# Kernel optimization log

Measured on AMD Instinct MI355X. Metric: run time of the kernel, lower is better.

## Reference

```python
import jax, jax.numpy as jnp
import numpy as np

B, S, D, O, R, E = 2, 4096, 4096, 4096, 256, 8
SCALE = 2.0

def setup_inputs() -> dict:
    key = jax.random.key(0)
    k_x, k_t, k_w, k_a, k_b = jax.random.split(key, 5)
    x = jax.random.normal(k_x, (B, S, D), dtype=jnp.float32)
    token_type = jax.random.randint(k_t, (S,), 0, E, dtype=jnp.int64)
    # weight_base: [out_features, in_features] as required by F.linear
    weight_base = jax.random.normal(k_w, (O, D), dtype=jnp.float32) * 0.02
    # LoRA stacks: lora_A [E, D, R], lora_B [E, R, O]. (Original inits B to zeros;
    # we use small random values so the LoRA path is numerically non-trivial.)
    lora_A = jax.random.normal(k_a, (E, D, R), dtype=jnp.float32) * 0.02
    lora_B = jax.random.normal(k_b, (E, R, O), dtype=jnp.float32) * 0.02
    return {"x": x, "weight_base": weight_base, "lora_A": lora_A,
            "lora_B": lora_B, "token_type": token_type}

def reference(x, weight_base, lora_A, lora_B, token_type):
    # base GEMM: F.linear(x, W) = x @ W.T  -> [B, S, O]
    base = jnp.einsum('bsd,od->bso', x, weight_base)
    # per-expert low-rank projection: h[e,b,s,:] = x[b,s,:] @ lora_A[e]
    h = jnp.einsum('bsd,edr->ebsr', x, lora_A)              # [E, B, S, R]
    # dispatch: zero out tokens not routed to expert e (token_type partitions S)
    onehot = jax.nn.one_hot(token_type, E, dtype=x.dtype)   # [S, E]
    h = h * onehot.T[:, None, :, None]                      # mask over (e, s)
    # combine: sum over experts of masked h @ lora_B[e]
    lora = jnp.einsum('ebsr,ero->bso', h, lora_B)           # [B, S, O]
    # every token has token_type in [0, E), so scatter covers all positions:
    # result = base + scale * expert_lora everywhere
    return base + SCALE * lora
```

## Files before the change

### kernel.cpp

```cpp
#include <hip/hip_runtime.h>

#define S_TOK 4096
#define D_DIM 4096
#define O_DIM 4096
#define R_DIM 256
#define E_EXP 8
#define NTOK  8192
#define KSPLIT 4

typedef __bf16 bf16x8 __attribute__((ext_vector_type(8)));
typedef float  f32x4  __attribute__((ext_vector_type(4)));

__device__ __forceinline__ unsigned short f2bf(float f) {
  unsigned int u = __float_as_uint(f);
  u += 0x7FFFu + ((u >> 16) & 1u);
  return (unsigned short)(u >> 16);
}
__device__ __forceinline__ float bf2f(unsigned short h) {
  return __uint_as_float(((unsigned int)h) << 16);
}

__device__ __forceinline__ void gload_lds16(const unsigned short* g, unsigned short* l) {
  __builtin_amdgcn_global_load_lds((const __attribute__((address_space(1))) void*)g,
                                   (__attribute__((address_space(3))) void*)l, 16, 0, 0);
}

#define PIPE_FENCE(N)                                                        \
  do {                                                                       \
    asm volatile("s_waitcnt vmcnt(" #N ")\n\ts_barrier" ::: "memory");       \
    __builtin_amdgcn_sched_barrier(0);                                       \
  } while (0)
#define LGKMC(N)                                                             \
  do {                                                                       \
    asm volatile("s_waitcnt lgkmcnt(" #N ")" ::: "memory");                  \
    __builtin_amdgcn_sched_barrier(0);                                       \
  } while (0)
#define SBAR0 __builtin_amdgcn_sched_barrier(0)

__global__ void cast8(const float* __restrict__ in, unsigned short* __restrict__ out) {
  size_t g = (size_t)blockIdx.x * 256 + threadIdx.x;
  const float4* i4 = (const float4*)in;
  float4 a = i4[g * 2], b = i4[g * 2 + 1];
  union { unsigned short h[8]; int4 v; } u;
  u.h[0] = f2bf(a.x); u.h[1] = f2bf(a.y); u.h[2] = f2bf(a.z); u.h[3] = f2bf(a.w);
  u.h[4] = f2bf(b.x); u.h[5] = f2bf(b.y); u.h[6] = f2bf(b.z); u.h[7] = f2bf(b.w);
  ((int4*)out)[g] = u.v;
}

__global__ void transpose_cast(const float* __restrict__ in, unsigned short* __restrict__ out,
                               int P, int Q) {
  __shared__ unsigned short tile[32][33];
  int e = blockIdx.z;
  int pt = blockIdx.x * 32, qt = blockIdx.y * 32;
  const float* ie = in + (size_t)e * P * Q;
  unsigned short* oe = out + (size_t)e * P * Q;
  int tx = threadIdx.x & 31, ty = threadIdx.x >> 5;
  #pragma unroll
  for (int i = 0; i < 32; i += 8) {
    int p = pt + ty + i, q = qt + tx;
    tile[ty + i][tx] = f2bf(ie[(size_t)p * Q + q]);
  }
  __syncthreads();
  #pragma unroll
  for (int i = 0; i < 32; i += 8) {
    int q = qt + ty + i, p = pt + tx;
    oe[(size_t)q * P + p] = tile[tx][ty + i];
  }
}

__global__ void sort_tokens(const int* __restrict__ tt, int* __restrict__ token_perm,
                            int* __restrict__ inv_perm,
                            int* __restrict__ tile_e, int* __restrict__ tile_j0,
                            int* __restrict__ tile_jend, int* __restrict__ ntiles_out) {
  __shared__ int ltt[S_TOK];
  __shared__ int lc[256 * 8];
  __shared__ int basee[8], cnte[8];
  __shared__ int ssl[S_TOK];
  int t = threadIdx.x;
  for (int s = t; s < S_TOK; s += 256) ltt[s] = tt[s];
  __syncthreads();
  int c[8] = {0,0,0,0,0,0,0,0};
  #pragma unroll
  for (int i = 0; i < 16; i++) { int e = ltt[t * 16 + i]; c[e]++; }
  #pragma unroll
  for (int e = 0; e < 8; e++) lc[t * 8 + e] = c[e];
  __syncthreads();
  if (t < 8) {
    int run = 0;
    for (int q = 0; q < 256; q++) { int tmp = lc[q * 8 + t]; lc[q * 8 + t] = run; run += tmp; }
    cnte[t] = run;
  }
  __syncthreads();
  if (t == 0) { int tot = 0; for (int e = 0; e < 8; e++) { basee[e] = tot; tot += cnte[e]; } }
  __syncthreads();
  int off[8];
  #pragma unroll
  for (int e = 0; e < 8; e++) off[e] = basee[e] + lc[t * 8 + e];
  #pragma unroll
  for (int i = 0; i < 16; i++) { int s = t * 16 + i; int e = ltt[s]; ssl[off[e]++] = s; }
  __syncthreads();
  for (int j = t; j < NTOK; j += 256) {
    int row = ((j & 1) << 12) + ssl[j >> 1];
    token_perm[j] = row;
    inv_perm[row] = j;
  }
  if (t == 0) {
    int nt = 0;
    for (int e = 0; e < 8; e++) {
      int js = 2 * basee[e], je = js + 2 * cnte[e];
      for (int j0 = js; j0 < je; j0 += 128) {
        tile_e[nt] = e; tile_j0[nt] = j0;
        tile_jend[nt] = (je < j0 + 128) ? je : (j0 + 128);
        nt++;
      }
    }
    *ntiles_out = nt;
  }
}

template<int FUSED>
__global__ __launch_bounds__(512, 2) void gemm256_dense(
    const unsigned short* __restrict__ A, const unsigned short* __restrict__ B,
    float* __restrict__ C, const unsigned short* __restrict__ lout,
    const int* __restrict__ invp) {
  __shared__ __align__(16) unsigned short ldsA[2][2][8192];
  __shared__ __align__(16) unsigned short ldsB[2][2][8192];
  int b = blockIdx.x;
  int xc = b & 7, q = b >> 3;
  const int bm = (xc >> 1) * 8 + (q >> 3);
  const int bn = (xc & 1) * 8 + (q & 7);
  const int tid = threadIdx.x, l = tid & 63, w = tid >> 6;
  const int wm = w >> 2, wn = w & 3;

  const unsigned short *srcA0, *srcA1, *srcB0, *srcB1;
  {
    int i0 = tid, r0 = i0 >> 2;
    int c0 = ((i0 & 3) * 16) ^ (((r0 >> 1) & 3) << 4);
    srcA0 = A + (size_t)(bm * 256 + r0) * 4096 + (c0 >> 1);
    srcB0 = B + (size_t)(bn * 256 + r0) * 4096 + (c0 >> 1);
    int i1 = 512 + tid, r1 = i1 >> 2;
    int c1 = ((i1 & 3) * 16) ^ (((r1 >> 1) & 3) << 4);
    srcA1 = A + (size_t)(bm * 256 + r1) * 4096 + (c1 >> 1);
    srcB1 = B + (size_t)(bn * 256 + r1) * 4096 + (c1 >> 1);
  }
  const int d0 = tid * 8;

  const int lane15 = l & 15, kb16 = (l >> 4) * 16;
  int offA[8], offB[4];
  #pragma unroll
  for (int m = 0; m < 8; m++) {
    int r = wm * 128 + m * 16 + lane15;
    offA[m] = r * 64 + (kb16 ^ (((r >> 1) & 3) << 4));
  }
  #pragma unroll
  for (int n = 0; n < 4; n++) {
    int r = wn * 64 + n * 16 + lane15;
    offB[n] = r * 64 + (kb16 ^ (((r >> 1) & 3) << 4));
  }

  f32x4 acc[8][4];
  #pragma unroll
  for (int m = 0; m < 8; m++)
    #pragma unroll
    for (int n = 0; n < 4; n++) acc[m][n] = (f32x4){0.f, 0.f, 0.f, 0.f};

  bf16x8 Ab0[4], Ab1[4], Bb0[4], Bb1[4];

#define STAGE_A(tt, kh) do { int _o = (tt) * 64 + (kh) * 32;                  \
    gload_lds16(srcA0 + _o, &ldsA[(tt) & 1][kh][d0]);                         \
    gload_lds16(srcA1 + _o, &ldsA[(tt) & 1][kh][d0 + 4096]); } while (0)
#define STAGE_B(tt, kh) do { int _o = (tt) * 64 + (kh) * 32;                  \
    gload_lds16(srcB0 + _o, &ldsB[(tt) & 1][kh][d0]);                         \
    gload_lds16(srcB1 + _o, &ldsB[(tt) & 1][kh][d0 + 4096]); } while (0)
#define RD_A(RING, QQ, KS, BUF) do {                                          \
    const char* _s = (const char*)&ldsA[RING][KS][0];                         \
    BUF[0] = *(const bf16x8*)(_s + offA[(QQ) * 4 + 0]);                       \
    BUF[1] = *(const bf16x8*)(_s + offA[(QQ) * 4 + 1]);                       \
    BUF[2] = *(const bf16x8*)(_s + offA[(QQ) * 4 + 2]);                       \
    BUF[3] = *(const bf16x8*)(_s + offA[(QQ) * 4 + 3]); } while (0)
#define RD_B(RING, KS, BUF) do {                                              \
    const char* _s = (const char*)&ldsB[RING][KS][0];                         \
    BUF[0] = *(const bf16x8*)(_s + offB[0]);                                  \
    BUF[1] = *(const bf16x8*)(_s + offB[1]);                                  \
    BUF[2] = *(const bf16x8*)(_s + offB[2]);                                  \
    BUF[3] = *(const bf16x8*)(_s + offB[3]); } while (0)
#define PRIO_MFMA(Q, AB, BB) do {                                             \
    __builtin_amdgcn_s_setprio(1);                                            \
    _Pragma("unroll")                                                         \
    for (int mm = 0; mm < 4; mm++)                                            \
      _Pragma("unroll")                                                       \
      for (int nn = 0; nn < 4; nn++)                                          \
        acc[(Q) * 4 + mm][nn] = __builtin_amdgcn_mfma_f32_16x16x32_bf16(      \
            AB[mm], BB[nn], acc[(Q) * 4 + mm][nn], 0, 0, 0);                  \
    __builtin_amdgcn_s_setprio(0); } while (0)

  STAGE_A(0, 0); STAGE_B(0, 0); STAGE_A(0, 1); STAGE_B(0, 1);
  STAGE_A(1, 0); STAGE_B(1, 0);
  PIPE_FENCE(4);
  RD_B(0, 0, Bb0); RD_A(0, 0, 0, Ab0);
  SBAR0;

  #pragma unroll 1
  for (int t = 0; t < 62; ++t) {
    const int r = t & 1, nr = r ^ 1;
    RD_A(r, 1, 0, Ab1); SBAR0; STAGE_A(t + 1, 1); SBAR0; LGKMC(4);
    PRIO_MFMA(0, Ab0, Bb0);
    RD_B(r, 1, Bb1); RD_A(r, 0, 1, Ab0); SBAR0; STAGE_B(t + 1, 1); SBAR0; LGKMC(8);
    PRIO_MFMA(1, Ab1, Bb0);
    PIPE_FENCE(4);
    RD_A(r, 1, 1, Ab1); SBAR0; STAGE_A(t + 2, 0); SBAR0; LGKMC(4);
    PRIO_MFMA(0, Ab0, Bb1);
    RD_B(nr, 0, Bb0); RD_A(nr, 0, 0, Ab0); SBAR0; STAGE_B(t + 2, 0); SBAR0; LGKMC(8);
    PRIO_MFMA(1, Ab1, Bb1);
    PIPE_FENCE(4);
  }
  RD_A(0, 1, 0, Ab1); SBAR0; STAGE_A(63, 1); SBAR0; LGKMC(4); PRIO_MFMA(0, Ab0, Bb0);
  RD_B(0, 1, Bb1); RD_A(0, 0, 1, Ab0); SBAR0; STAGE_B(63, 1); SBAR0; LGKMC(8);
  PRIO_MFMA(1, Ab1, Bb0); PIPE_FENCE(4);
  RD_A(0, 1, 1, Ab1); SBAR0; LGKMC(4); PRIO_MFMA(0, Ab0, Bb1);
  RD_B(1, 0, Bb0); RD_A(1, 0, 0, Ab0); SBAR0; LGKMC(8); PRIO_MFMA(1, Ab1, Bb1);
  PIPE_FENCE(0);
  RD_A(1, 1, 0, Ab1); SBAR0; LGKMC(4); PRIO_MFMA(0, Ab0, Bb0);
  RD_B(1, 1, Bb1); RD_A(1, 0, 1, Ab0); SBAR0; LGKMC(8); PRIO_MFMA(1, Ab1, Bb0);
  RD_A(1, 1, 1, Ab1); SBAR0; LGKMC(4); PRIO_MFMA(0, Ab0, Bb1);
  LGKMC(0); PRIO_MFMA(1, Ab1, Bb1);

#undef STAGE_A
#undef STAGE_B
#undef RD_A
#undef RD_B
#undef PRIO_MFMA

  const int rowbase = bm * 256 + wm * 128;
  const int colbase = bn * 256 + wn * 64;
  #pragma unroll
  for (int m = 0; m < 8; m++)
    #pragma unroll
    for (int v = 0; v < 4; v++) {
      int rrow = rowbase + m * 16 + (l >> 4) * 4 + v;
      float lv0 = 0.f, lv1 = 0.f, lv2 = 0.f, lv3 = 0.f;
      if (FUSED) {
        int jr = invp[rrow];
        const unsigned short* lr = lout + (size_t)jr * O_DIM + colbase + lane15;
        lv0 = bf2f(lr[0]); lv1 = bf2f(lr[16]); lv2 = bf2f(lr[32]); lv3 = bf2f(lr[48]);
      }
      size_t base = (size_t)rrow * O_DIM + colbase + lane15;
      C[base]      = acc[m][0][v] + lv0;
      C[base + 16] = acc[m][1][v] + lv1;
      C[base + 32] = acc[m][2][v] + lv2;
      C[base + 48] = acc[m][3][v] + lv3;
    }
}

template<int MODE>
__global__ __launch_bounds__(256, 2) void gemm_nt(
    const unsigned short* __restrict__ Aop, const unsigned short* __restrict__ Bop,
    float* __restrict__ outF, unsigned short* __restrict__ outU,
    const int* __restrict__ perm, const int* __restrict__ tile_e,
    const int* __restrict__ tile_j0, const int* __restrict__ tile_jend,
    const int* __restrict__ ntiles, int K) {
  int bm = blockIdx.x, bn = blockIdx.y;
  if (bm >= *ntiles) return;
  int e = tile_e[bm], j0 = tile_j0[bm], jend = tile_jend[bm];
  const int kc = (MODE == 1) ? blockIdx.z : 0;
  const int t = threadIdx.x;
  const int l = t & 63, w = t >> 6;
  __shared__ __align__(16) unsigned short lA[128 * 32];
  __shared__ __align__(16) unsigned short lB[128 * 32];

  const unsigned short* srcA[2];
  const unsigned short* srcB[2];
  #pragma unroll
  for (int ck = 0; ck < 2; ck++) {
    int idx = t + ck * 256;
    int lrow = idx >> 2, lk = (idx & 3) * 8;
    int j = j0 + lrow; if (j > jend - 1) j = jend - 1;
    int grow = (MODE == 1) ? perm[j] : j;
    srcA[ck] = Aop + (size_t)grow * K + lk + kc * 1024;
    int bcol = bn * 128 + lrow;
    const unsigned short* bp = Bop;
    if (MODE == 1) bp += (size_t)e * R_DIM * D_DIM;
    else           bp += (size_t)e * O_DIM * R_DIM;
    srcB[ck] = bp + (size_t)bcol * K + lk + kc * 1024;
  }

  f32x4 acc[4][4];
  #pragma unroll
  for (int m = 0; m < 4; m++)
    #pragma unroll
    for (int n = 0; n < 4; n++) acc[m][n] = (f32x4){0.f, 0.f, 0.f, 0.f};

  const int wr = w >> 1, wc = w & 1;
  const int ra = wr * 64 + (l & 15);
  const int rb = wc * 64 + (l & 15);
  const int ko = (l >> 4) * 8;

  const int nk = (MODE == 1) ? (1024 / 32) : (K / 32);
  for (int kt = 0; kt < nk; kt++) {
    __syncthreads();
    #pragma unroll
    for (int ck = 0; ck < 2; ck++) {
      gload_lds16(srcA[ck] + kt * 32, &lA[(w * 64 + ck * 256) * 8]);
      gload_lds16(srcB[ck] + kt * 32, &lB[(w * 64 + ck * 256) * 8]);
    }
    __syncthreads();
    bf16x8 af[4], bfr[4];
    #pragma unroll
    for (int m = 0; m < 4; m++) af[m] = *(const bf16x8*)&lA[(ra + m * 16) * 32 + ko];
    #pragma unroll
    for (int n = 0; n < 4; n++) bfr[n] = *(const bf16x8*)&lB[(rb + n * 16) * 32 + ko];
    #pragma unroll
    for (int m = 0; m < 4; m++)
      #pragma unroll
      for (int n = 0; n < 4; n++)
        acc[m][n] = __builtin_amdgcn_mfma_f32_16x16x32_bf16(af[m], bfr[n], acc[m][n], 0, 0, 0);
  }

  int rowbase = j0 + wr * 64;
  int colbase = bn * 128 + wc * 64;
  #pragma unroll
  for (int m = 0; m < 4; m++) {
    #pragma unroll
    for (int n = 0; n < 4; n++) {
      #pragma unroll
      for (int v = 0; v < 4; v++) {
        int r = rowbase + m * 16 + (l >> 4) * 4 + v;
        int cc = colbase + n * 16 + (l & 15);
        if (r < jend) {
          if (MODE == 1) {
            outU[(size_t)kc * (NTOK * R_DIM) + (size_t)r * R_DIM + cc] = f2bf(acc[m][n][v]);
          } else if (MODE == 2) {
            size_t o = (size_t)perm[r] * O_DIM + cc;
            outF[o] += 2.0f * acc[m][n][v];
          } else {
            outU[(size_t)r * O_DIM + cc] = f2bf(2.0f * acc[m][n][v]);
          }
        }
      }
    }
  }
}

__global__ void reduce_h(const unsigned short* __restrict__ hp, unsigned short* __restrict__ h16) {
  size_t g = (size_t)blockIdx.x * 256 + threadIdx.x;
  float s[8] = {0,0,0,0,0,0,0,0};
  #pragma unroll
  for (int c = 0; c < KSPLIT; c++) {
    int4 v = ((const int4*)hp)[g + (size_t)c * (NTOK * R_DIM / 8)];
    const unsigned short* us = (const unsigned short*)&v;
    #pragma unroll
    for (int i = 0; i < 8; i++) s[i] += bf2f(us[i]);
  }
  union { unsigned short h[8]; int4 v; } u;
  #pragma unroll
  for (int i = 0; i < 8; i++) u.h[i] = f2bf(s[i]);
  ((int4*)h16)[g] = u.v;
}

#define X16_OFF   ((size_t)0)
#define W16_OFF   ((size_t)67108864)
#define A16T_OFF  ((size_t)100663296)
#define B16T_OFF  ((size_t)117440512)
#define H16S_OFF  ((size_t)134217728)
#define PERM_OFF  ((size_t)138412032)
#define INVP_OFF  ((size_t)138444800)
#define TILEE_OFF ((size_t)138477568)
#define TILEJ0_OFF ((size_t)138478080)
#define TILEJE_OFF ((size_t)138478592)
#define NT_OFF    ((size_t)138479104)
#define HP16_OFF  ((size_t)138479616)
#define LOUT_OFF  ((size_t)155256832)
#define WS_FUSED_NEED ((size_t)222365696)

extern "C" void kernel_launch(void* const* d_in, const int* in_sizes, int n_in,
                              void* d_out, int out_size, void* d_ws, size_t ws_size,
                              hipStream_t stream) {
  const float* x  = (const float*)d_in[0];
  const float* wb = (const float*)d_in[1];
  const float* la = (const float*)d_in[2];
  const float* lb = (const float*)d_in[3];
  const int* tok  = (const int*)d_in[4];
  float* out = (float*)d_out;

  char* ws = (char*)d_ws;
  unsigned short* X16  = (unsigned short*)(ws + X16_OFF);
  unsigned short* W16  = (unsigned short*)(ws + W16_OFF);
  unsigned short* A16t = (unsigned short*)(ws + A16T_OFF);
  unsigned short* B16t = (unsigned short*)(ws + B16T_OFF);
  unsigned short* H16s = (unsigned short*)(ws + H16S_OFF);
  int* perm  = (int*)(ws + PERM_OFF);
  int* invp  = (int*)(ws + INVP_OFF);
  int* tl_e  = (int*)(ws + TILEE_OFF);
  int* tl_j0 = (int*)(ws + TILEJ0_OFF);
  int* tl_je = (int*)(ws + TILEJE_OFF);
  int* nt    = (int*)(ws + NT_OFF);

  const bool fused = ws_size >= WS_FUSED_NEED;

  cast8<<<16384, 256, 0, stream>>>(x, X16);
  cast8<<<8192, 256, 0, stream>>>(wb, W16);
  transpose_cast<<<dim3(128, 8, 8), 256, 0, stream>>>(la, A16t, D_DIM, R_DIM);
  transpose_cast<<<dim3(8, 128, 8), 256, 0, stream>>>(lb, B16t, R_DIM, O_DIM);
  sort_tokens<<<1, 256, 0, stream>>>(tok, perm, invp, tl_e, tl_j0, tl_je, nt);

  if (fused) {
    unsigned short* HP16 = (unsigned short*)(ws + HP16_OFF);
    unsigned short* LOUT = (unsigned short*)(ws + LOUT_OFF);
    gemm_nt<1><<<dim3(71, 2, KSPLIT), 256, 0, stream>>>(X16, A16t, nullptr, HP16,
                                                        perm, tl_e, tl_j0, tl_je, nt, D_DIM);
    reduce_h<<<1024, 256, 0, stream>>>(HP16, H16s);
    gemm_nt<3><<<dim3(71, 32), 256, 0, stream>>>(H16s, B16t, nullptr, LOUT,
                                                 perm, tl_e, tl_j0, tl_je, nt, R_DIM);
    gemm256_dense<1><<<512, 512, 0, stream>>>(X16, W16, out, LOUT, invp);
  } else {
    unsigned short* HP16 = (unsigned short*)(ws + W16_OFF);
    gemm256_dense<0><<<512, 512, 0, stream>>>(X16, W16, out, nullptr, nullptr);
    gemm_nt<1><<<dim3(71, 2, KSPLIT), 256, 0, stream>>>(X16, A16t, nullptr, HP16,
                                                        perm, tl_e, tl_j0, tl_je, nt, D_DIM);
    reduce_h<<<1024, 256, 0, stream>>>(HP16, H16s);
    gemm_nt<2><<<dim3(71, 32), 256, 0, stream>>>(H16s, B16t, out, nullptr,
                                                 perm, tl_e, tl_j0, tl_je, nt, R_DIM);
  }
}
```

Baseline: 456.9 us.

## Pipeline LoRA GEMMs with 4-stage LDS ring and merge prologue cast kernels

Rewrites the grouped LoRA GEMM kernel to use a 4-deep LDS ring buffer with asynchronous global-to-LDS loads, XOR-swizzled LDS layout, and a single barrier per k-step. It also raises MFMA wave priority, replacing the old two-barrier, unpipelined loop. The four cast/transpose kernels are merged into one prologue launch, and the non-fused fallback path is removed. Larger LDS use (64KB per block) may reduce occupancy, and the fallback removal assumes the workspace is always large enough.

```diff
diff --git a/kernel.cpp b/kernel.cpp
--- a/kernel.cpp
+++ b/kernel.cpp
@@ -37,24 +37,37 @@
   } while (0)
 #define SBAR0 __builtin_amdgcn_sched_barrier(0)
 
-__global__ void cast8(const float* __restrict__ in, unsigned short* __restrict__ out) {
-  size_t g = (size_t)blockIdx.x * 256 + threadIdx.x;
-  const float4* i4 = (const float4*)in;
-  float4 a = i4[g * 2], b = i4[g * 2 + 1];
-  union { unsigned short h[8]; int4 v; } u;
-  u.h[0] = f2bf(a.x); u.h[1] = f2bf(a.y); u.h[2] = f2bf(a.z); u.h[3] = f2bf(a.w);
-  u.h[4] = f2bf(b.x); u.h[5] = f2bf(b.y); u.h[6] = f2bf(b.z); u.h[7] = f2bf(b.w);
-  ((int4*)out)[g] = u.v;
-}
-
-__global__ void transpose_cast(const float* __restrict__ in, unsigned short* __restrict__ out,
-                               int P, int Q) {
+__global__ void prologue(const float* __restrict__ x, const float* __restrict__ wb,
+                         const float* __restrict__ la, const float* __restrict__ lb,
+                         unsigned short* __restrict__ X16, unsigned short* __restrict__ W16,
+                         unsigned short* __restrict__ A16t, unsigned short* __restrict__ B16t) {
   __shared__ unsigned short tile[32][33];
-  int e = blockIdx.z;
-  int pt = blockIdx.x * 32, qt = blockIdx.y * 32;
+  const int b = blockIdx.x, t = threadIdx.x;
+  if (b < 24576) {
+    const float* in  = (b < 16384) ? x : wb;
+    unsigned short* out = (b < 16384) ? X16 : W16;
+    size_t g = (size_t)((b < 16384) ? b : (b - 16384)) * 256 + t;
+    const float4* i4 = (const float4*)in;
+    float4 a = i4[g * 2], c = i4[g * 2 + 1];
+    union { unsigned short h[8]; int4 v; } u;
+    u.h[0] = f2bf(a.x); u.h[1] = f2bf(a.y); u.h[2] = f2bf(a.z); u.h[3] = f2bf(a.w);
+    u.h[4] = f2bf(c.x); u.h[5] = f2bf(c.y); u.h[6] = f2bf(c.z); u.h[7] = f2bf(c.w);
+    ((int4*)out)[g] = u.v;
+    return;
+  }
+  const float* in; unsigned short* out; int P, Q, pt, qt, e;
+  if (b < 32768) {
+    int b2 = b - 24576; e = b2 >> 10; int rem = b2 & 1023;
+    in = la; out = A16t; P = D_DIM; Q = R_DIM;
+    pt = (rem >> 3) * 32; qt = (rem & 7) * 32;
+  } else {
+    int b3 = b - 32768; e = b3 >> 10; int rem = b3 & 1023;
+    in = lb; out = B16t; P = R_DIM; Q = D_DIM;
+    pt = (rem & 7) * 32; qt = (rem >> 3) * 32;
+  }
   const float* ie = in + (size_t)e * P * Q;
   unsigned short* oe = out + (size_t)e * P * Q;
-  int tx = threadIdx.x & 31, ty = threadIdx.x >> 5;
+  int tx = t & 31, ty = t >> 5;
   #pragma unroll
   for (int i = 0; i < 32; i += 8) {
     int p = pt + ty + i, q = qt + tx;
@@ -255,7 +268,7 @@
 template<int MODE>
 __global__ __launch_bounds__(256, 2) void gemm_nt(
     const unsigned short* __restrict__ Aop, const unsigned short* __restrict__ Bop,
-    float* __restrict__ outF, unsigned short* __restrict__ outU,
+    unsigned short* __restrict__ outU,
     const int* __restrict__ perm, const int* __restrict__ tile_e,
     const int* __restrict__ tile_j0, const int* __restrict__ tile_jend,
     const int* __restrict__ ntiles, int K) {
@@ -263,25 +276,41 @@
   if (bm >= *ntiles) return;
   int e = tile_e[bm], j0 = tile_j0[bm], jend = tile_jend[bm];
   const int kc = (MODE == 1) ? blockIdx.z : 0;
-  const int t = threadIdx.x;
-  const int l = t & 63, w = t >> 6;
-  __shared__ __align__(16) unsigned short lA[128 * 32];
-  __shared__ __align__(16) unsigned short lB[128 * 32];
-
-  const unsigned short* srcA[2];
-  const unsigned short* srcB[2];
-  #pragma unroll
-  for (int ck = 0; ck < 2; ck++) {
-    int idx = t + ck * 256;
-    int lrow = idx >> 2, lk = (idx & 3) * 8;
-    int j = j0 + lrow; if (j > jend - 1) j = jend - 1;
-    int grow = (MODE == 1) ? perm[j] : j;
-    srcA[ck] = Aop + (size_t)grow * K + lk + kc * 1024;
-    int bcol = bn * 128 + lrow;
-    const unsigned short* bp = Bop;
-    if (MODE == 1) bp += (size_t)e * R_DIM * D_DIM;
-    else           bp += (size_t)e * O_DIM * R_DIM;
-    srcB[ck] = bp + (size_t)bcol * K + lk + kc * 1024;
+  const int t = threadIdx.x, l = t & 63, w = t >> 6;
+  const int wm = w >> 1, wn = w & 1;
+  __shared__ __align__(16) unsigned short ldsA[4][4096];
+  __shared__ __align__(16) unsigned short ldsB[4][4096];
+
+  const unsigned short *sA0, *sA1, *sB0, *sB1;
+  {
+    int i0 = t, r0 = i0 >> 2;
+    int c0 = ((i0 & 3) * 16) ^ (((r0 >> 1) & 3) << 4);
+    int i1 = 256 + t, r1 = i1 >> 2;
+    int c1 = ((i1 & 3) * 16) ^ (((r1 >> 1) & 3) << 4);
+    int ja = j0 + r0; if (ja > jend - 1) ja = jend - 1;
+    int jb = j0 + r1; if (jb > jend - 1) jb = jend - 1;
+    int g0 = (MODE == 1) ? perm[ja] : ja;
+    int g1 = (MODE == 1) ? perm[jb] : jb;
+    sA0 = Aop + (size_t)g0 * K + kc * 1024 + (c0 >> 1);
+    sA1 = Aop + (size_t)g1 * K + kc * 1024 + (c1 >> 1);
+    const unsigned short* bp = Bop + ((MODE == 1) ? (size_t)e * R_DIM * D_DIM
+                                                  : (size_t)e * O_DIM * R_DIM);
+    sB0 = bp + (size_t)(bn * 128 + r0) * K + kc * 1024 + (c0 >> 1);
+    sB1 = bp + (size_t)(bn * 128 + r1) * K + kc * 1024 + (c1 >> 1);
+  }
+  const int d0 = t * 8;
+
+  const int lane15 = l & 15, kb16 = (l >> 4) * 16;
+  int offA[4], offB[4];
+  #pragma unroll
+  for (int m = 0; m < 4; m++) {
+    int r = wm * 64 + m * 16 + lane15;
+    offA[m] = r * 64 + (kb16 ^ (((r >> 1) & 3) << 4));
+  }
+  #pragma unroll
+  for (int n = 0; n < 4; n++) {
+    int r = wn * 64 + n * 16 + lane15;
+    offB[n] = r * 64 + (kb16 ^ (((r >> 1) & 3) << 4));
   }
 
   f32x4 acc[4][4];
@@ -290,34 +319,49 @@
     #pragma unroll
     for (int n = 0; n < 4; n++) acc[m][n] = (f32x4){0.f, 0.f, 0.f, 0.f};
 
-  const int wr = w >> 1, wc = w & 1;
-  const int ra = wr * 64 + (l & 15);
-  const int rb = wc * 64 + (l & 15);
-  const int ko = (l >> 4) * 8;
-
-  const int nk = (MODE == 1) ? (1024 / 32) : (K / 32);
-  for (int kt = 0; kt < nk; kt++) {
-    __syncthreads();
-    #pragma unroll
-    for (int ck = 0; ck < 2; ck++) {
-      gload_lds16(srcA[ck] + kt * 32, &lA[(w * 64 + ck * 256) * 8]);
-      gload_lds16(srcB[ck] + kt * 32, &lB[(w * 64 + ck * 256) * 8]);
-    }
-    __syncthreads();
-    bf16x8 af[4], bfr[4];
-    #pragma unroll
-    for (int m = 0; m < 4; m++) af[m] = *(const bf16x8*)&lA[(ra + m * 16) * 32 + ko];
-    #pragma unroll
-    for (int n = 0; n < 4; n++) bfr[n] = *(const bf16x8*)&lB[(rb + n * 16) * 32 + ko];
+  auto stage = [&](int tt) {
+    const int ring = tt & 3;
+    const int go = tt * 32;
+    gload_lds16(sA0 + go, &ldsA[ring][d0]);
+    gload_lds16(sA1 + go, &ldsA[ring][d0 + 2048]);
+    gload_lds16(sB0 + go, &ldsB[ring][d0]);
+    gload_lds16(sB1 + go, &ldsB[ring][d0 + 2048]);
+  };
+
+  auto body = [&](int ring) {
+    const char* bA = (const char*)&ldsA[ring][0];
+    const char* bB = (const char*)&ldsB[ring][0];
+    bf16x8 a[4], bb[4];
+    #pragma unroll
+    for (int m = 0; m < 4; m++) a[m] = *(const bf16x8*)(bA + offA[m]);
+    #pragma unroll
+    for (int n = 0; n < 4; n++) bb[n] = *(const bf16x8*)(bB + offB[n]);
+    __builtin_amdgcn_s_setprio(1);
     #pragma unroll
     for (int m = 0; m < 4; m++)
       #pragma unroll
       for (int n = 0; n < 4; n++)
-        acc[m][n] = __builtin_amdgcn_mfma_f32_16x16x32_bf16(af[m], bfr[n], acc[m][n], 0, 0, 0);
-  }
-
-  int rowbase = j0 + wr * 64;
-  int colbase = bn * 128 + wc * 64;
+        acc[m][n] = __builtin_amdgcn_mfma_f32_16x16x32_bf16(a[m], bb[n], acc[m][n], 0, 0, 0);
+    __builtin_amdgcn_s_setprio(0);
+  };
+
+  const int nk = (MODE == 1) ? 32 : (K / 32);
+  stage(0); stage(1); stage(2);
+  PIPE_FENCE(8);
+  #pragma unroll 1
+  for (int kt = 0; kt < nk - 3; ++kt) {
+    stage(kt + 3);
+    body(kt & 3);
+    PIPE_FENCE(8);
+  }
+  body((nk - 3) & 3);
+  PIPE_FENCE(4);
+  body((nk - 2) & 3);
+  PIPE_FENCE(0);
+  body((nk - 1) & 3);
+
+  const int rowbase = j0 + wm * 64;
+  const int colbase = bn * 128 + wn * 64;
   #pragma unroll
   for (int m = 0; m < 4; m++) {
     #pragma unroll
@@ -325,13 +369,10 @@
       #pragma unroll
       for (int v = 0; v < 4; v++) {
         int r = rowbase + m * 16 + (l >> 4) * 4 + v;
-        int cc = colbase + n * 16 + (l & 15);
+        int cc = colbase + n * 16 + lane15;
         if (r < jend) {
           if (MODE == 1) {
             outU[(size_t)kc * (NTOK * R_DIM) + (size_t)r * R_DIM + cc] = f2bf(acc[m][n][v]);
-          } else if (MODE == 2) {
-            size_t o = (size_t)perm[r] * O_DIM + cc;
-            outF[o] += 2.0f * acc[m][n][v];
           } else {
             outU[(size_t)r * O_DIM + cc] = f2bf(2.0f * acc[m][n][v]);
           }
@@ -370,7 +411,7 @@
 #define NT_OFF    ((size_t)138479104)
 #define HP16_OFF  ((size_t)138479616)
 #define LOUT_OFF  ((size_t)155256832)
-#define WS_FUSED_NEED ((size_t)222365696)
+#define WS_NEED   ((size_t)222365696)
 
 extern "C" void kernel_launch(void* const* d_in, const int* in_sizes, int n_in,
                               void* d_out, int out_size, void* d_ws, size_t ws_size,
@@ -388,6 +429,8 @@
   unsigned short* A16t = (unsigned short*)(ws + A16T_OFF);
   unsigned short* B16t = (unsigned short*)(ws + B16T_OFF);
   unsigned short* H16s = (unsigned short*)(ws + H16S_OFF);
+  unsigned short* HP16 = (unsigned short*)(ws + HP16_OFF);
+  unsigned short* LOUT = (unsigned short*)(ws + LOUT_OFF);
   int* perm  = (int*)(ws + PERM_OFF);
   int* invp  = (int*)(ws + INVP_OFF);
   int* tl_e  = (int*)(ws + TILEE_OFF);
@@ -395,30 +438,13 @@
   int* tl_je = (int*)(ws + TILEJE_OFF);
   int* nt    = (int*)(ws + NT_OFF);
 
-  const bool fused = ws_size >= WS_FUSED_NEED;
-
-  cast8<<<16384, 256, 0, stream>>>(x, X16);
-  cast8<<<8192, 256, 0, stream>>>(wb, W16);
-  transpose_cast<<<dim3(128, 8, 8), 256, 0, stream>>>(la, A16t, D_DIM, R_DIM);
-  transpose_cast<<<dim3(8, 128, 8), 256, 0, stream>>>(lb, B16t, R_DIM, O_DIM);
+  prologue<<<40960, 256, 0, stream>>>(x, wb, la, lb, X16, W16, A16t, B16t);
   sort_tokens<<<1, 256, 0, stream>>>(tok, perm, invp, tl_e, tl_j0, tl_je, nt);
 
-  if (fused) {
-    unsigned short* HP16 = (unsigned short*)(ws + HP16_OFF);
-    unsigned short* LOUT = (unsigned short*)(ws + LOUT_OFF);
-    gemm_nt<1><<<dim3(71, 2, KSPLIT), 256, 0, stream>>>(X16, A16t, nullptr, HP16,
-                                                        perm, tl_e, tl_j0, tl_je, nt, D_DIM);
-    reduce_h<<<1024, 256, 0, stream>>>(HP16, H16s);
-    gemm_nt<3><<<dim3(71, 32), 256, 0, stream>>>(H16s, B16t, nullptr, LOUT,
-                                                 perm, tl_e, tl_j0, tl_je, nt, R_DIM);
-    gemm256_dense<1><<<512, 512, 0, stream>>>(X16, W16, out, LOUT, invp);
-  } else {
-    unsigned short* HP16 = (unsigned short*)(ws + W16_OFF);
-    gemm256_dense<0><<<512, 512, 0, stream>>>(X16, W16, out, nullptr, nullptr);
-    gemm_nt<1><<<dim3(71, 2, KSPLIT), 256, 0, stream>>>(X16, A16t, nullptr, HP16,
-                                                        perm, tl_e, tl_j0, tl_je, nt, D_DIM);
-    reduce_h<<<1024, 256, 0, stream>>>(HP16, H16s);
-    gemm_nt<2><<<dim3(71, 32), 256, 0, stream>>>(H16s, B16t, out, nullptr,
-                                                 perm, tl_e, tl_j0, tl_je, nt, R_DIM);
-  }
-}
+  gemm_nt<1><<<dim3(71, 2, KSPLIT), 256, 0, stream>>>(X16, A16t, HP16,
+                                                      perm, tl_e, tl_j0, tl_je, nt, D_DIM);
+  reduce_h<<<1024, 256, 0, stream>>>(HP16, H16s);
+  gemm_nt<3><<<dim3(71, 32), 256, 0, stream>>>(H16s, B16t, LOUT,
+                                               perm, tl_e, tl_j0, tl_je, nt, R_DIM);
+  gemm256_dense<1><<<512, 512, 0, stream>>>(X16, W16, out, LOUT, invp);
+}
```

Result: no change. 459.0 us (+0.5%).
